# Performance work log

Hardware: AMD Instinct MI355X
Metric: run time of the kernel (lower is better)

## Reference

```python
import jax, jax.numpy as jnp
import numpy as np

B, C, H, W = 2, 256, 48, 48
NH = 8
HD = C // NH  # 32
T = H * W    # 2304


def setup_inputs() -> dict:
    keys = jax.random.split(jax.random.key(0), 16)
    s = lambda fan: 1.0 / np.sqrt(fan)
    x = jax.random.normal(keys[0], (B, C, H, W), jnp.float32)
    wq = jax.random.normal(keys[1], (C, C), jnp.float32) * s(C)
    bq = jax.random.normal(keys[2], (C,), jnp.float32) * 0.01
    wk = jax.random.normal(keys[3], (C, C), jnp.float32) * s(C)
    bk = jax.random.normal(keys[4], (C,), jnp.float32) * 0.01
    wv = jax.random.normal(keys[5], (C, C), jnp.float32) * s(C)
    bv = jax.random.normal(keys[6], (C,), jnp.float32) * 0.01
    wo = jax.random.normal(keys[7], (C, C), jnp.float32) * s(C)
    bo = jax.random.normal(keys[8], (C,), jnp.float32) * 0.01
    gamma1 = jnp.ones((C,), jnp.float32)
    beta1 = jnp.zeros((C,), jnp.float32)
    w1 = jax.random.normal(keys[9], (4 * C, C), jnp.float32) * s(C)
    bf1 = jax.random.normal(keys[10], (4 * C,), jnp.float32) * 0.01
    w2 = jax.random.normal(keys[11], (C, 4 * C), jnp.float32) * s(4 * C)
    bf2 = jax.random.normal(keys[12], (C,), jnp.float32) * 0.01
    gamma2 = jnp.ones((C,), jnp.float32)
    beta2 = jnp.zeros((C,), jnp.float32)
    return dict(x=x, wq=wq, bq=bq, wk=wk, bk=bk, wv=wv, bv=bv, wo=wo, bo=bo,
                gamma1=gamma1, beta1=beta1, w1=w1, bf1=bf1, w2=w2, bf2=bf2,
                gamma2=gamma2, beta2=beta2)


def group_norm1(x, gamma, beta, eps=1e-5):
    # GroupNorm(1, C): normalize over (C, H, W) per sample, per-channel affine.
    mu = jnp.mean(x, axis=(1, 2, 3), keepdims=True)
    var = jnp.mean((x - mu) ** 2, axis=(1, 2, 3), keepdims=True)
    xn = (x - mu) * jax.lax.rsqrt(var + eps)
    return xn * gamma[None, :, None, None] + beta[None, :, None, None]


def reference(x, wq, bq, wk, bk, wv, bv, wo, bo, gamma1, beta1,
              w1, bf1, w2, bf2, gamma2, beta2):
    b, c, h, w = x.shape
    t = h * w
    xt = x.reshape(b, c, t).transpose(0, 2, 1)  # [b, t, c]
    # 1x1 conv == per-token linear
    def heads(y):
        return y.reshape(b, t, NH, HD).transpose(0, 2, 1, 3)  # [b, nh, t, hd]
    q = heads(xt @ wq.T + bq)
    k = heads(xt @ wk.T + bk)
    v = heads(xt @ wv.T + bv)
    # flash SDPA runs in fp16 with fp32 accumulation
    q16 = q.astype(jnp.float16)
    k16 = k.astype(jnp.float16)
    v16 = v.astype(jnp.float16)
    scale = 1.0 / np.sqrt(HD)
    scores = jnp.einsum('bhqd,bhkd->bhqk', q16.astype(jnp.float32),
                        k16.astype(jnp.float32)) * scale
    attn = jax.nn.softmax(scores, axis=-1)
    out = jnp.einsum('bhqk,bhkd->bhqd', attn,
                     v16.astype(jnp.float32)).astype(jnp.float16)
    # remove component along normalized v (fp16, like torch code)
    vn = v16 / jnp.maximum(
        jnp.sqrt(jnp.sum(v16 * v16, axis=-1, keepdims=True)),
        jnp.float16(1e-12))
    out = out - jnp.sum(out * vn, axis=-1, keepdims=True) * vn
    out = out.astype(x.dtype)
    out = out.transpose(0, 2, 1, 3).reshape(b, t, c)  # [b, t, c]
    out = out @ wo.T + bo
    out = out.transpose(0, 2, 1).reshape(b, c, h, w)
    x1 = group_norm1(x + out, gamma1, beta1)
    # FFN: 1x1 conv -> relu -> 1x1 conv, per token
    x1t = x1.reshape(b, c, t).transpose(0, 2, 1)  # [b, t, c]
    hdn = jax.nn.relu(x1t @ w1.T + bf1)
    ffn = (hdn @ w2.T + bf2).transpose(0, 2, 1).reshape(b, c, h, w)
    x2 = group_norm1(x1 + ffn, gamma2, beta2)
    return x2
```

## Files before the change

kernel.cpp:

```cpp
#include <hip/hip_runtime.h>
#include <hip/hip_fp16.h>

typedef _Float16 f16x8 __attribute__((ext_vector_type(8)));
typedef float f32x4 __attribute__((ext_vector_type(4)));

namespace {

constexpr int B = 2, C = 256, T = 2304, F = 1024, NH = 8, HD = 32;
constexpr int BH = B * NH;
constexpr int NCHUNK = 4;
constexpr int CHUNK = T / NCHUNK;
constexpr float C2 = 0.17677669529663687f * 1.4426950408889634f;
constexpr float INV_N = 1.0f / (float)(C * T);

constexpr size_t N_WQKV = (size_t)3 * C * C;
constexpr size_t N_WO   = (size_t)C * C;
constexpr size_t N_W1   = (size_t)F * C;
constexpr size_t N_W2   = (size_t)C * F;
constexpr size_t N_WALL = N_WQKV + N_WO + N_W1 + N_W2;

constexpr size_t OFF_QKV  = 0;
constexpr size_t SZ_QKV   = (size_t)B * 3 * C * T * 2;
constexpr size_t OFF_AO   = OFF_QKV + SZ_QKV;
constexpr size_t SZ_AO    = (size_t)B * C * T * 2;
constexpr size_t OFF_X1   = OFF_AO + SZ_AO;
constexpr size_t SZ_X1    = (size_t)B * C * T * 4;
constexpr size_t OFF_PART = OFF_X1 + SZ_X1;
constexpr size_t SZ_OP    = (size_t)NCHUNK * BH * HD * T * 2;
constexpr size_t SZ_MP    = (size_t)NCHUNK * BH * T * 4;
constexpr size_t OFF_OP   = OFF_PART;
constexpr size_t OFF_MP   = OFF_OP + SZ_OP;
constexpr size_t OFF_LP   = OFF_MP + SZ_MP;
constexpr size_t SZ_H16   = (size_t)B * F * T * 2;
constexpr size_t SZ_PART  = SZ_OP + 2 * SZ_MP;
constexpr size_t SZ_UNION = SZ_PART > SZ_H16 ? SZ_PART : SZ_H16;
constexpr size_t OFF_H16  = OFF_PART;
constexpr size_t OFF_W16  = OFF_PART + SZ_UNION;
constexpr size_t OFF_BQKV = OFF_W16 + N_WALL * 2;
constexpr size_t OFF_STATS = OFF_BQKV + (size_t)3 * C * 4;

}

__global__ __launch_bounds__(256)
void convert_weights(const float* __restrict__ wq, const float* __restrict__ wk,
                     const float* __restrict__ wv, const float* __restrict__ wo,
                     const float* __restrict__ w1, const float* __restrict__ w2,
                     const float* __restrict__ bq, const float* __restrict__ bk,
                     const float* __restrict__ bv,
                     _Float16* __restrict__ w16, float* __restrict__ bqkv,
                     float* __restrict__ stats)
{
  const size_t tid = (size_t)blockIdx.x * 256 + threadIdx.x;
  if (tid < 8) stats[tid] = 0.f;
  if (tid < 3 * C)
    bqkv[tid] = tid < C ? bq[tid] : (tid < 2 * C ? bk[tid - C] : bv[tid - 2 * C]);
  for (size_t i = tid; i < N_WALL; i += (size_t)gridDim.x * 256) {
    float v;
    if      (i < 65536)  v = wq[i];
    else if (i < 131072) v = wk[i - 65536];
    else if (i < 196608) v = wv[i - 131072];
    else if (i < 262144) v = wo[i - 196608];
    else if (i < 524288) v = w1[i - 262144];
    else                 v = w2[i - 524288];
    w16[i] = (_Float16)v;
  }
}

template<bool RELU, bool RES, bool GNIN, bool GNRES, bool STATS,
         typename InT, typename OutT>
__global__ __launch_bounds__(256)
void gemm_mfma(const _Float16* __restrict__ W, const InT* __restrict__ X,
               const float* __restrict__ bias, const float* __restrict__ res,
               OutT* __restrict__ out, int CO, int K,
               const float* __restrict__ stats_in,
               const float* __restrict__ gamma, const float* __restrict__ beta,
               float* __restrict__ stats_out)
{
  const int b   = blockIdx.z;
  const int co0 = blockIdx.y * 64;
  const int t0  = blockIdx.x * 64;
  const int tid = threadIdx.x;
  const int wid = tid >> 6, lane = tid & 63;
  const int g = lane >> 4, lo = lane & 15;
  const int wm = wid & 1, wn = wid >> 1;

  __shared__ f16x8 xs[2][4][64];
  __shared__ float gs[256], bs[256];
  __shared__ float red[8];

  float mu = 0.f, rsig = 0.f;
  if (GNIN || GNRES) {
    const float s1 = stats_in[b * 2], s2 = stats_in[b * 2 + 1];
    mu = s1 * INV_N;
    rsig = rsqrtf(s2 * INV_N - mu * mu + 1e-5f);
  }
  if (GNIN) { gs[tid] = gamma[tid]; bs[tid] = beta[tid]; }

  const f32x4 z4 = {0.f, 0.f, 0.f, 0.f};
  f32x4 acc00 = z4, acc01 = z4, acc10 = z4, acc11 = z4;

  const int st = tid & 63;
  const int kp = tid >> 6;
  const InT* Xp = X + (size_t)b * K * T + t0 + st;
  const _Float16* Wp = W + (size_t)(co0 + wm * 32 + lo) * K + 8 * g;

  float xr[8];
#pragma unroll
  for (int j = 0; j < 8; ++j) xr[j] = (float)Xp[(size_t)(kp * 8 + j) * T];

  __syncthreads();

  int it = 0;
  for (int k0 = 0; k0 < K; k0 += 32, ++it) {
    const int buf = it & 1;
    f16x8 wv_;
#pragma unroll
    for (int j = 0; j < 8; ++j) {
      float v = xr[j];
      if (GNIN) { const int k = k0 + kp * 8 + j; v = (v - mu) * rsig * gs[k] + bs[k]; }
      wv_[j] = (_Float16)v;
    }
    xs[buf][kp][st] = wv_;

    const int k1 = (k0 + 32 < K) ? k0 + 32 : k0;
#pragma unroll
    for (int j = 0; j < 8; ++j) xr[j] = (float)Xp[(size_t)(k1 + kp * 8 + j) * T];

    __syncthreads();

    const f16x8 af0 = *(const f16x8*)(Wp + (size_t)k0);
    const f16x8 af1 = *(const f16x8*)(Wp + (size_t)16 * K + k0);
    const f16x8 bf0 = xs[buf][g][wn * 32 + lo];
    const f16x8 bf1 = xs[buf][g][wn * 32 + 16 + lo];
    acc00 = __builtin_amdgcn_mfma_f32_16x16x32_f16(af0, bf0, acc00, 0, 0, 0);
    acc01 = __builtin_amdgcn_mfma_f32_16x16x32_f16(af0, bf1, acc01, 0, 0, 0);
    acc10 = __builtin_amdgcn_mfma_f32_16x16x32_f16(af1, bf0, acc10, 0, 0, 0);
    acc11 = __builtin_amdgcn_mfma_f32_16x16x32_f16(af1, bf1, acc11, 0, 0, 0);
  }

  float s = 0.f, ss = 0.f;
  const size_t obase = ((size_t)b * CO + co0 + wm * 32) * T + t0 + wn * 32 + lo;
  const float* resb = res + obase;
  OutT* outb = out + obase;
  const f32x4 accs[2][2] = {{acc00, acc01}, {acc10, acc11}};
#pragma unroll
  for (int mi = 0; mi < 2; ++mi) {
#pragma unroll
    for (int r = 0; r < 4; ++r) {
      const int row = mi * 16 + 4 * g + r;
      const int co = co0 + wm * 32 + row;
      const float bi = bias[co];
      float gm = 0.f, bt = 0.f;
      if (GNRES) { gm = gamma[co]; bt = beta[co]; }
#pragma unroll
      for (int ni = 0; ni < 2; ++ni) {
        float v = accs[mi][ni][r] + bi;
        if (RES) {
          float rv = resb[(size_t)row * T + ni * 16];
          if (GNRES) rv = (rv - mu) * rsig * gm + bt;
          v += rv;
        }
        if (RELU) v = fmaxf(v, 0.f);
        outb[(size_t)row * T + ni * 16] = (OutT)v;
        if (STATS) { s += v; ss = fmaf(v, v, ss); }
      }
    }
  }

  if (STATS) {
#pragma unroll
    for (int off = 32; off > 0; off >>= 1) {
      s  += __shfl_down(s, off);
      ss += __shfl_down(ss, off);
    }
    if (lane == 0) { red[wid] = s; red[4 + wid] = ss; }
    __syncthreads();
    if (tid == 0) {
      atomicAdd(&stats_out[b * 2],     red[0] + red[1] + red[2] + red[3]);
      atomicAdd(&stats_out[b * 2 + 1], red[4] + red[5] + red[6] + red[7]);
    }
  }
}

__global__ __launch_bounds__(512)
void attn_mfma(const _Float16* __restrict__ qkv, _Float16* __restrict__ opart,
               float* __restrict__ mpart, float* __restrict__ lpart)
{
  const int tid  = threadIdx.x;
  const int wid  = tid >> 6;
  const int lane = tid & 63;
  const int g    = lane >> 4;
  const int lo   = lane & 15;
  const int chunk = blockIdx.y;
  const int bh   = blockIdx.z;
  const int b    = bh >> 3, h = bh & 7;
  const int tq   = blockIdx.x * 128 + wid * 16 + lo;
  const size_t qb = ((size_t)b * 3 * C + h * HD) * T;
  const size_t kb = qb + (size_t)C * T;
  const size_t vb = qb + (size_t)2 * C * T;

  __shared__ _Float16 kt[2][64][36];
  __shared__ _Float16 vt[2][32][72];
  __shared__ _Float16 pl[8][16][72];

  const int t   = tid & 63;
  const int dp  = tid >> 6;
  const int dv  = tid >> 4;
  const int seg = tid & 15;

  f16x8 qf;
#pragma unroll
  for (int j = 0; j < 8; ++j)
    qf[j] = (_Float16)((float)qkv[qb + (size_t)(8 * g + j) * T + tq] * C2);

  const f32x4 zero4 = {0.f, 0.f, 0.f, 0.f};
  f32x4 oa[2] = {zero4, zero4};
  float m = -1e30f, l = 0.f;

  constexpr int NIT = CHUNK / 64;

  ushort ka[4];
  uint2  va;
  {
    const int tk0 = chunk * CHUNK;
#pragma unroll
    for (int dd = 0; dd < 4; ++dd)
      ka[dd] = *(const ushort*)(qkv + kb + (size_t)(dp * 4 + dd) * T + tk0 + t);
    va = *(const uint2*)(qkv + vb + (size_t)dv * T + tk0 + seg * 4);
  }

  for (int it = 0; it < NIT; ++it) {
    const int buf = it & 1;

    *(uint*)&kt[buf][t][dp * 4]     = (uint)ka[0] | ((uint)ka[1] << 16);
    *(uint*)&kt[buf][t][dp * 4 + 2] = (uint)ka[2] | ((uint)ka[3] << 16);
    *(uint2*)&vt[buf][dv][seg * 4] = va;

    {
      const int tkn = chunk * CHUNK + (it + 1 < NIT ? it + 1 : it) * 64;
      ushort ka2[4];
      uint2  va2;
#pragma unroll
      for (int dd = 0; dd < 4; ++dd)
        ka2[dd] = *(const ushort*)(qkv + kb + (size_t)(dp * 4 + dd) * T + tkn + t);
      va2 = *(const uint2*)(qkv + vb + (size_t)dv * T + tkn + seg * 4);

      __syncthreads();

      f32x4 s4[4];
#pragma unroll
      for (int mt = 0; mt < 4; ++mt) {
        union { f16x8 v; uint2 u[2]; } kf;
        const _Float16* kr = &kt[buf][mt * 16 + lo][8 * g];
        kf.u[0] = *(const uint2*)(kr);
        kf.u[1] = *(const uint2*)(kr + 4);
        s4[mt] = __builtin_amdgcn_mfma_f32_16x16x32_f16(kf.v, qf, zero4, 0, 0, 0);
      }
      float rmax = -1e30f;
#pragma unroll
      for (int mt = 0; mt < 4; ++mt) {
        const float m01 = fmaxf(s4[mt][0], s4[mt][1]);
        const float m23 = fmaxf(s4[mt][2], s4[mt][3]);
        rmax = fmaxf(rmax, fmaxf(m01, m23));
      }
      rmax = fmaxf(rmax, __shfl_xor(rmax, 16));
      rmax = fmaxf(rmax, __shfl_xor(rmax, 32));
      const float mn = fmaxf(m, rmax);
      const float fsc = __builtin_amdgcn_exp2f(m - mn);
      m = mn;
      float p[4][4];
      float psum = 0.f;
#pragma unroll
      for (int mt = 0; mt < 4; ++mt)
#pragma unroll
        for (int r = 0; r < 4; ++r) {
          p[mt][r] = __builtin_amdgcn_exp2f(s4[mt][r] - mn);
          psum += p[mt][r];
        }
      psum += __shfl_xor(psum, 16);
      psum += __shfl_xor(psum, 32);
      l = l * fsc + psum;
#pragma unroll
      for (int dt = 0; dt < 2; ++dt)
#pragma unroll
        for (int r = 0; r < 4; ++r) oa[dt][r] *= fsc;

#pragma unroll
      for (int mt = 0; mt < 4; ++mt) {
        union { _Float16 e[4]; uint2 u2; } pw;
#pragma unroll
        for (int r = 0; r < 4; ++r) pw.e[r] = (_Float16)p[mt][r];
        *(uint2*)&pl[wid][lo][16 * mt + 4 * g] = pw.u2;
      }
#pragma unroll
      for (int c2 = 0; c2 < 2; ++c2) {
        const f16x8 pbv = *(const f16x8*)&pl[wid][lo][c2 * 32 + 8 * g];
#pragma unroll
        for (int dt = 0; dt < 2; ++dt) {
          const f16x8 vf = *(const f16x8*)&vt[buf][dt * 16 + lo][c2 * 32 + 8 * g];
          oa[dt] = __builtin_amdgcn_mfma_f32_16x16x32_f16(vf, pbv, oa[dt], 0, 0, 0);
        }
      }

#pragma unroll
      for (int dd = 0; dd < 4; ++dd) ka[dd] = ka2[dd];
      va = va2;
    }
  }

  const float invL = 1.f / l;
  const size_t ob = (size_t)(chunk * BH + bh) * HD * T;
#pragma unroll
  for (int dt = 0; dt < 2; ++dt)
#pragma unroll
    for (int r = 0; r < 4; ++r)
      opart[ob + (size_t)(dt * 16 + 4 * g + r) * T + tq] =
          (_Float16)(oa[dt][r] * invL);
  if (g == 0) {
    const size_t pb = (size_t)(chunk * BH + bh) * T + tq;
    mpart[pb] = m;
    lpart[pb] = l;
  }
}

__global__ __launch_bounds__(64)
void attn_combine(const _Float16* __restrict__ opart, const float* __restrict__ mpart,
                  const float* __restrict__ lpart, const _Float16* __restrict__ qkv,
                  _Float16* __restrict__ AOh)
{
  const int q  = blockIdx.x * 64 + threadIdx.x;
  const int bh = blockIdx.y;
  const int b  = bh >> 3, h = bh & 7;
  float mv[NCHUNK], lv[NCHUNK];
  float M = -1e30f;
#pragma unroll
  for (int c = 0; c < NCHUNK; ++c) {
    const size_t pb = (size_t)(c * BH + bh) * T + q;
    mv[c] = mpart[pb];
    lv[c] = lpart[pb];
    M = fmaxf(M, mv[c]);
  }
  float L = 0.f;
  float wc[NCHUNK];
#pragma unroll
  for (int c = 0; c < NCHUNK; ++c) {
    wc[c] = __builtin_amdgcn_exp2f(mv[c] - M) * lv[c];
    L += wc[c];
  }
  const float inv = 1.f / L;
#pragma unroll
  for (int c = 0; c < NCHUNK; ++c) wc[c] *= inv;

  float o[HD];
#pragma unroll
  for (int d = 0; d < HD; ++d) o[d] = 0.f;
#pragma unroll
  for (int c = 0; c < NCHUNK; ++c) {
    const size_t ob = (size_t)(c * BH + bh) * HD * T + q;
#pragma unroll
    for (int d = 0; d < HD; ++d)
      o[d] = fmaf(wc[c], (float)opart[ob + (size_t)d * T], o[d]);
  }

  const size_t vbase = ((size_t)b * 3 * C + 2 * C + h * HD) * T + q;
  float vv[HD], nrm2 = 0.f;
#pragma unroll
  for (int d = 0; d < HD; ++d) {
    vv[d] = (float)qkv[vbase + (size_t)d * T];
    nrm2 = fmaf(vv[d], vv[d], nrm2);
  }
  const float nrm = fmaxf(sqrtf(nrm2), 1e-12f);
  float dot = 0.f;
  float o16[HD], vn[HD];
#pragma unroll
  for (int d = 0; d < HD; ++d) {
    o16[d] = (float)(_Float16)(o[d]);
    vn[d]  = (float)(_Float16)(vv[d] / nrm);
    dot = fmaf(o16[d], vn[d], dot);
  }
  const size_t ab = ((size_t)b * C + h * HD) * T + q;
#pragma unroll
  for (int d = 0; d < HD; ++d)
    AOh[ab + (size_t)d * T] = (_Float16)(o16[d] - dot * vn[d]);
}

__global__ __launch_bounds__(256)
void gn_norm(const float* __restrict__ Y, const float* __restrict__ stats,
             const float* __restrict__ gamma, const float* __restrict__ beta,
             float* __restrict__ O)
{
  const int i = blockIdx.x * 256 + threadIdx.x;
  const int b = i / (C * T);
  const int c = (i / T) & (C - 1);
  const float mu  = stats[b * 2] * INV_N;
  const float var = stats[b * 2 + 1] * INV_N - mu * mu;
  const float r = rsqrtf(var + 1e-5f);
  O[i] = (Y[i] - mu) * r * gamma[c] + beta[c];
}

extern "C" void kernel_launch(void* const* d_in, const int* in_sizes, int n_in,
                              void* d_out, int out_size, void* d_ws, size_t ws_size,
                              hipStream_t stream)
{
  const float* x      = (const float*)d_in[0];
  const float* wq     = (const float*)d_in[1];
  const float* bq     = (const float*)d_in[2];
  const float* wk     = (const float*)d_in[3];
  const float* bk     = (const float*)d_in[4];
  const float* wv     = (const float*)d_in[5];
  const float* bv     = (const float*)d_in[6];
  const float* wo     = (const float*)d_in[7];
  const float* bo     = (const float*)d_in[8];
  const float* gamma1 = (const float*)d_in[9];
  const float* beta1  = (const float*)d_in[10];
  const float* w1     = (const float*)d_in[11];
  const float* bf1    = (const float*)d_in[12];
  const float* w2     = (const float*)d_in[13];
  const float* bf2    = (const float*)d_in[14];
  const float* gamma2 = (const float*)d_in[15];
  const float* beta2  = (const float*)d_in[16];

  char* ws = (char*)d_ws;
  _Float16* qkv16 = (_Float16*)(ws + OFF_QKV);
  _Float16* ao16  = (_Float16*)(ws + OFF_AO);
  float*    x1    = (float*)(ws + OFF_X1);
  _Float16* opart = (_Float16*)(ws + OFF_OP);
  float*    mpart = (float*)(ws + OFF_MP);
  float*    lpart = (float*)(ws + OFF_LP);
  _Float16* h16   = (_Float16*)(ws + OFF_H16);
  _Float16* w16   = (_Float16*)(ws + OFF_W16);
  float*    bqkv  = (float*)(ws + OFF_BQKV);
  float*    stats = (float*)(ws + OFF_STATS);
  float*    out   = (float*)d_out;

  const _Float16* wqkv16 = w16;
  const _Float16* wo16   = w16 + N_WQKV;
  const _Float16* w116   = w16 + N_WQKV + N_WO;
  const _Float16* w216   = w16 + N_WQKV + N_WO + N_W1;

  const dim3 blk256(256);

  convert_weights<<<768, blk256, 0, stream>>>(wq, wk, wv, wo, w1, w2, bq, bk, bv,
                                              w16, bqkv, stats);

  gemm_mfma<false, false, false, false, false, float, _Float16>
      <<<dim3(36, 12, 2), blk256, 0, stream>>>(
          wqkv16, x, bqkv, nullptr, qkv16, 3 * C, C, nullptr, nullptr, nullptr, nullptr);

  attn_mfma<<<dim3(T / 128, NCHUNK, BH), dim3(512), 0, stream>>>(qkv16, opart, mpart, lpart);
  attn_combine<<<dim3(T / 64, BH), dim3(64), 0, stream>>>(opart, mpart, lpart, qkv16, ao16);

  gemm_mfma<false, true, false, false, true, _Float16, float>
      <<<dim3(36, 4, 2), blk256, 0, stream>>>(
          wo16, ao16, bo, x, x1, C, C, nullptr, nullptr, nullptr, stats);

  gemm_mfma<true, false, true, false, false, float, _Float16>
      <<<dim3(36, 16, 2), blk256, 0, stream>>>(
          w116, x1, bf1, nullptr, h16, F, C, stats, gamma1, beta1, nullptr);

  gemm_mfma<false, true, false, true, true, _Float16, float>
      <<<dim3(36, 4, 2), blk256, 0, stream>>>(
          w216, h16, bf2, x1, out, C, F, stats, gamma1, beta1, stats + 4);

  gn_norm<<<dim3(4608), blk256, 0, stream>>>(out, stats + 4, gamma2, beta2, out);
}
```

Baseline: 125.9 us.

## Prefetch GEMM weight fragments, skip unneeded softmax rescale, pack fp16 conversions

The GEMM kernel now loads the next K-slice's weight fragments into registers one iteration ahead, so global loads overlap the MFMA work. The flash-attention loop skips the running-max rescale of l and the output accumulators when no lane's new row max exceeds the current max. Scalar fp16 conversions are replaced by packed round-toward-zero cvt_pkrtz in the GEMM input staging and the P-matrix write, and weight conversion now uses float4 loads. Round-toward-zero changes fp16 rounding slightly, and the prefetch raises register pressure.

```diff
diff --git a/kernel.cpp b/kernel.cpp
--- a/kernel.cpp
+++ b/kernel.cpp
@@ -2,6 +2,7 @@
 #include <hip/hip_fp16.h>
 
 typedef _Float16 f16x8 __attribute__((ext_vector_type(8)));
+typedef __fp16 fp16x2 __attribute__((ext_vector_type(2)));
 typedef float f32x4 __attribute__((ext_vector_type(4)));
 
 namespace {
@@ -54,15 +55,20 @@
   if (tid < 8) stats[tid] = 0.f;
   if (tid < 3 * C)
     bqkv[tid] = tid < C ? bq[tid] : (tid < 2 * C ? bk[tid - C] : bv[tid - 2 * C]);
-  for (size_t i = tid; i < N_WALL; i += (size_t)gridDim.x * 256) {
-    float v;
-    if      (i < 65536)  v = wq[i];
-    else if (i < 131072) v = wk[i - 65536];
-    else if (i < 196608) v = wv[i - 131072];
-    else if (i < 262144) v = wo[i - 196608];
-    else if (i < 524288) v = w1[i - 262144];
-    else                 v = w2[i - 524288];
-    w16[i] = (_Float16)v;
+  for (size_t i4 = tid; i4 < N_WALL / 4; i4 += (size_t)gridDim.x * 256) {
+    const size_t e = i4 * 4;
+    const float* src;
+    if      (e < 65536)  src = wq + e;
+    else if (e < 131072) src = wk + (e - 65536);
+    else if (e < 196608) src = wv + (e - 131072);
+    else if (e < 262144) src = wo + (e - 196608);
+    else if (e < 524288) src = w1 + (e - 262144);
+    else                 src = w2 + (e - 524288);
+    const float4 v = *(const float4*)src;
+    union { _Float16 h[4]; uint2 u; } pk;
+    pk.h[0] = (_Float16)v.x; pk.h[1] = (_Float16)v.y;
+    pk.h[2] = (_Float16)v.z; pk.h[3] = (_Float16)v.w;
+    *(uint2*)(w16 + e) = pk.u;
   }
 }
 
@@ -107,35 +113,44 @@
   float xr[8];
 #pragma unroll
   for (int j = 0; j < 8; ++j) xr[j] = (float)Xp[(size_t)(kp * 8 + j) * T];
+  f16x8 afc0 = *(const f16x8*)(Wp);
+  f16x8 afc1 = *(const f16x8*)(Wp + (size_t)16 * K);
 
   __syncthreads();
 
   int it = 0;
   for (int k0 = 0; k0 < K; k0 += 32, ++it) {
     const int buf = it & 1;
-    f16x8 wv_;
-#pragma unroll
-    for (int j = 0; j < 8; ++j) {
-      float v = xr[j];
-      if (GNIN) { const int k = k0 + kp * 8 + j; v = (v - mu) * rsig * gs[k] + bs[k]; }
-      wv_[j] = (_Float16)v;
+    union { fp16x2 h2[4]; f16x8 v8; } u;
+#pragma unroll
+    for (int j2 = 0; j2 < 4; ++j2) {
+      float v0 = xr[2 * j2], v1 = xr[2 * j2 + 1];
+      if (GNIN) {
+        const int k = k0 + kp * 8 + 2 * j2;
+        v0 = (v0 - mu) * rsig * gs[k] + bs[k];
+        v1 = (v1 - mu) * rsig * gs[k + 1] + bs[k + 1];
+      }
+      u.h2[j2] = __builtin_amdgcn_cvt_pkrtz(v0, v1);
     }
-    xs[buf][kp][st] = wv_;
+    xs[buf][kp][st] = u.v8;
 
     const int k1 = (k0 + 32 < K) ? k0 + 32 : k0;
 #pragma unroll
     for (int j = 0; j < 8; ++j) xr[j] = (float)Xp[(size_t)(k1 + kp * 8 + j) * T];
+    const f16x8 afn0 = *(const f16x8*)(Wp + (size_t)k1);
+    const f16x8 afn1 = *(const f16x8*)(Wp + (size_t)16 * K + k1);
 
     __syncthreads();
 
-    const f16x8 af0 = *(const f16x8*)(Wp + (size_t)k0);
-    const f16x8 af1 = *(const f16x8*)(Wp + (size_t)16 * K + k0);
     const f16x8 bf0 = xs[buf][g][wn * 32 + lo];
     const f16x8 bf1 = xs[buf][g][wn * 32 + 16 + lo];
-    acc00 = __builtin_amdgcn_mfma_f32_16x16x32_f16(af0, bf0, acc00, 0, 0, 0);
-    acc01 = __builtin_amdgcn_mfma_f32_16x16x32_f16(af0, bf1, acc01, 0, 0, 0);
-    acc10 = __builtin_amdgcn_mfma_f32_16x16x32_f16(af1, bf0, acc10, 0, 0, 0);
-    acc11 = __builtin_amdgcn_mfma_f32_16x16x32_f16(af1, bf1, acc11, 0, 0, 0);
+    acc00 = __builtin_amdgcn_mfma_f32_16x16x32_f16(afc0, bf0, acc00, 0, 0, 0);
+    acc01 = __builtin_amdgcn_mfma_f32_16x16x32_f16(afc0, bf1, acc01, 0, 0, 0);
+    acc10 = __builtin_amdgcn_mfma_f32_16x16x32_f16(afc1, bf0, acc10, 0, 0, 0);
+    acc11 = __builtin_amdgcn_mfma_f32_16x16x32_f16(afc1, bf1, acc11, 0, 0, 0);
+
+    afc0 = afn0;
+    afc1 = afn1;
   }
 
   float s = 0.f, ss = 0.f;
@@ -265,31 +280,34 @@
       }
       rmax = fmaxf(rmax, __shfl_xor(rmax, 16));
       rmax = fmaxf(rmax, __shfl_xor(rmax, 32));
-      const float mn = fmaxf(m, rmax);
-      const float fsc = __builtin_amdgcn_exp2f(m - mn);
-      m = mn;
+      if (!__all(rmax <= m)) {
+        const float mn = fmaxf(m, rmax);
+        const float fsc = __builtin_amdgcn_exp2f(m - mn);
+        m = mn;
+        l *= fsc;
+#pragma unroll
+        for (int dt = 0; dt < 2; ++dt)
+#pragma unroll
+          for (int r = 0; r < 4; ++r) oa[dt][r] *= fsc;
+      }
       float p[4][4];
       float psum = 0.f;
 #pragma unroll
       for (int mt = 0; mt < 4; ++mt)
 #pragma unroll
         for (int r = 0; r < 4; ++r) {
-          p[mt][r] = __builtin_amdgcn_exp2f(s4[mt][r] - mn);
+          p[mt][r] = __builtin_amdgcn_exp2f(s4[mt][r] - m);
           psum += p[mt][r];
         }
       psum += __shfl_xor(psum, 16);
       psum += __shfl_xor(psum, 32);
-      l = l * fsc + psum;
-#pragma unroll
-      for (int dt = 0; dt < 2; ++dt)
-#pragma unroll
-        for (int r = 0; r < 4; ++r) oa[dt][r] *= fsc;
+      l += psum;
 
 #pragma unroll
       for (int mt = 0; mt < 4; ++mt) {
-        union { _Float16 e[4]; uint2 u2; } pw;
-#pragma unroll
-        for (int r = 0; r < 4; ++r) pw.e[r] = (_Float16)p[mt][r];
+        union { fp16x2 h2[2]; uint2 u2; } pw;
+        pw.h2[0] = __builtin_amdgcn_cvt_pkrtz(p[mt][0], p[mt][1]);
+        pw.h2[1] = __builtin_amdgcn_cvt_pkrtz(p[mt][2], p[mt][3]);
         *(uint2*)&pl[wid][lo][16 * mt + 4 * g] = pw.u2;
       }
 #pragma unroll
```

Result: no change. 125.3 us (-0.4%).
